# Kernel optimization log

Hardware: AMD Instinct MI355X
Metric: run time of the kernel (lower is better)

## Reference

```python
import jax, jax.numpy as jnp
import numpy as np

B, L, H, N, CH = 8, 2048, 512, 64, 1


def setup_inputs() -> dict:
    key = jax.random.key(0)
    ks = jax.random.split(key, 7)
    # S4D-Lin style init: w = -0.5 + i*pi*n, with slight noise on the real part
    w_re = -(0.5 + 0.1 * jax.random.uniform(ks[0], (H, N), dtype=jnp.float32))
    w_im = jnp.broadcast_to(jnp.pi * jnp.arange(N, dtype=jnp.float32), (H, N)).copy()
    C_re = jax.random.normal(ks[1], (CH, H, N), dtype=jnp.float32)
    C_im = jax.random.normal(ks[2], (CH, H, N), dtype=jnp.float32)
    D = jax.random.normal(ks[3], (CH, H), dtype=jnp.float32)
    # log-uniform dt in [1e-3, 1e-1]
    log_dt = jax.random.uniform(ks[4], (H,), dtype=jnp.float32,
                                minval=jnp.log(1e-3), maxval=jnp.log(1e-1))
    dt = jnp.exp(log_dt)
    u = jax.random.normal(ks[5], (B, L, H), dtype=jnp.float32)
    return {"u": u, "w_re": w_re, "w_im": w_im, "C_re": C_re,
            "C_im": C_im, "D": D, "dt": dt}


def reference(u, w_re, w_im, C_re, C_im, D, dt):
    # u: [B, L, H] -> [B, H, L]
    uT = jnp.swapaxes(u, -1, -2)
    l = uT.shape[-1]
    h = dt.shape[-1]
    w = (w_re + 1j * w_im).astype(jnp.complex64)          # [t, n]
    v = h // w.shape[0]
    w = jnp.tile(w, (v, 1))                                # [h, n]
    C = (C_re + 1j * C_im).astype(jnp.complex64)           # [c, h, n]
    # --- kernel generation ---
    dtA = w * dt[:, None]                                  # [h, n]
    K = jnp.arange(l) * dtA[..., None]                     # [h, n, l]
    Cs = C * ((jnp.exp(dtA) - 1.0) / w)                    # [c, h, n]
    k = 2.0 * jnp.einsum('chn,hnl->chl', Cs, jnp.exp(K)).real  # [c, h, l]
    # --- FFT convolution ---
    k_f = jnp.fft.rfft(k, n=2 * l - 1)                     # [c, h, l]
    u_f = jnp.fft.rfft(uT, n=2 * l - 1)                    # [B, h, l]
    y_f = jnp.einsum('...hl,chl->...chl', u_f, k_f)        # [B, c, h, l]
    y = jnp.fft.irfft(y_f, n=2 * l)[..., :l]               # [B, c, h, l]
    # skip connection
    y = y + jnp.einsum('...hl,ch->...chl', uT, D)
    # '... c h l -> ... l c h'
    return jnp.moveaxis(y, (-3, -2, -1), (-2, -1, -3))
```

## Files before the change

### kernel.cpp

```cpp
#include <hip/hip_runtime.h>
#include <hip/hip_bf16.h>
#include <math.h>


namespace {
constexpr int cB = 8;
constexpr int cL = 2048;
constexpr int cH = 512;
constexpr int cN = 64;
constexpr int M1 = 4095;
constexpr int M2 = 4096;
constexpr int BH = cB * cH;
constexpr int MA = BH + cH;

constexpr size_t S0   = 2 * ((size_t)cH * cN * 6);
constexpr size_t S_B1 = S0;
constexpr size_t S_A  = S_B1 + (size_t)4096 * 2048;
constexpr size_t S_T2 = S_A  + (size_t)MA * 2048;
constexpr size_t S_U  = S_T2 + (size_t)2048 * 4096;
}

typedef __attribute__((ext_vector_type(8))) short short8;
typedef __attribute__((ext_vector_type(4))) short sh4;
typedef __attribute__((ext_vector_type(4))) float f32x4;

static __device__ inline short f2bf(float x) {
    __hip_bfloat16 h = __float2bfloat16(x);
    return *reinterpret_cast<short*>(&h);
}
static __device__ inline float bf2f(short s) {
    return __uint_as_float(((unsigned int)(unsigned short)s) << 16);
}
static __device__ __forceinline__ void load_lds16(const short* g, short* l) {
    __builtin_amdgcn_global_load_lds(
        (const __attribute__((address_space(1))) void*)g,
        (__attribute__((address_space(3))) void*)l, 16, 0, 0);
}
#define WAIT_LGKM0() do { asm volatile("s_waitcnt lgkmcnt(0)" ::: "memory"); \
                          __builtin_amdgcn_sched_barrier(0); } while (0)
#define WAIT_VM(n)   do { asm volatile("s_waitcnt vmcnt(" #n ")" ::: "memory"); \
                          __builtin_amdgcn_sched_barrier(0); } while (0)
#define BAR() __builtin_amdgcn_s_barrier()

__global__ __launch_bounds__(256) void k_tabs(short* __restrict__ Wb)
{
    int tid = threadIdx.x;
    if (blockIdx.x < 2048) {
        int j  = blockIdx.x;
        int t0 = tid * 8;
        int p0 = (int)(((long)j * t0) % M1);
        float c, s, cs, ss;
        sincosf((6.283185307179586f / (float)M1) * (float)p0, &s, &c);
        sincosf((6.283185307179586f / (float)M1) * (float)j,  &ss, &cs);
        short8 vc, vs;
#pragma unroll
        for (int i = 0; i < 8; ++i) {
            vc[i] = f2bf(c); vs[i] = f2bf(s);
            float tr = c * cs - s * ss;
            s = c * ss + s * cs;
            c = tr;
        }
        *(short8*)&Wb[S_B1 + (size_t)(2 * j)     * 2048 + t0] = vc;
        *(short8*)&Wb[S_B1 + (size_t)(2 * j + 1) * 2048 + t0] = vs;
    } else {
        int t  = blockIdx.x - 2048;
        int j0 = tid * 8;
        int p0 = (t * j0) & (M2 - 1);
        float c, s, cs, ss;
        sincosf((6.283185307179586f / (float)M2) * (float)p0, &s, &c);
        sincosf((6.283185307179586f / (float)M2) * (float)t,  &ss, &cs);
        short8 vc, vs;
#pragma unroll
        for (int i = 0; i < 8; ++i) {
            vc[i] = f2bf(c); vs[i] = f2bf(s);
            float tr = c * cs - s * ss;
            s = c * ss + s * cs;
            c = tr;
        }
        *(short8*)&Wb[S_T2 + (size_t)t * 4096 + j0]        = vc;
        *(short8*)&Wb[S_T2 + (size_t)t * 4096 + 2048 + j0] = vs;
    }
}

__global__ __launch_bounds__(256) void k_trans(const float* __restrict__ u,
                                               short* __restrict__ Wb)
{
    __shared__ float tile[64][65];
    int t0 = blockIdx.x * 64;
    int h0 = blockIdx.y * 64;
    int b  = blockIdx.z;
    int cx = threadIdx.x & 63, r0 = threadIdx.x >> 6;
#pragma unroll
    for (int i = 0; i < 16; ++i) {
        int row = r0 + i * 4;
        tile[row][cx] = u[((size_t)b * cL + t0 + row) * cH + h0 + cx];
    }
    __syncthreads();
    short* A = Wb + S_A;
#pragma unroll
    for (int i = 0; i < 16; ++i) {
        int hrow = r0 + i * 4;
        A[(size_t)(b * cH + h0 + hrow) * 2048 + t0 + cx] = f2bf(tile[cx][hrow]);
    }
}

__global__ __launch_bounds__(256) void k_kgen(
    const float* __restrict__ w_re, const float* __restrict__ w_im,
    const float* __restrict__ C_re, const float* __restrict__ C_im,
    const float* __restrict__ dt, short* __restrict__ Wb)
{
    __shared__ float md[cN * 6];
    int h = blockIdx.x, tid = threadIdx.x;
    if (tid < cN) {
        int idx = h * cN + tid;
        double dtv = dt[h];
        double wr = w_re[idx], wi = w_im[idx];
        double ar = wr * dtv, ai = wi * dtv;
        double er = exp(ar);
        double zs, zc; sincos(ai, &zs, &zc);
        double zr = er * zc, zi = er * zs;
        double nr = zr - 1.0, ni = zi;
        double inv = 1.0 / (wr * wr + wi * wi);
        double gr = (nr * wr + ni * wi) * inv;
        double gi = (ni * wr - nr * wi) * inv;
        double cr = C_re[idx], ci = C_im[idx];
        md[tid*6+0] = (float)(cr * gr - ci * gi);
        md[tid*6+1] = (float)(cr * gi + ci * gr);
        md[tid*6+2] = (float)zr; md[tid*6+3] = (float)zi;
        md[tid*6+4] = (float)ar; md[tid*6+5] = (float)ai;
    }
    __syncthreads();
    int t0 = tid * 8;
    float acc[8] = {0.f, 0.f, 0.f, 0.f, 0.f, 0.f, 0.f, 0.f};
    for (int n = 0; n < cN; ++n) {
        float csr = md[n*6+0], csi = md[n*6+1];
        float zr  = md[n*6+2], zi  = md[n*6+3];
        float ar  = md[n*6+4], ai  = md[n*6+5];
        float mag = expf(ar * (float)t0);
        double ph = fmod((double)ai * (double)t0, 6.283185307179586);
        float s, c; sincosf((float)ph, &s, &c);
        float pr = mag * c, pi = mag * s;
#pragma unroll
        for (int i = 0; i < 8; ++i) {
            acc[i] += csr * pr - csi * pi;
            float tr = pr * zr - pi * zi;
            pi = pr * zi + pi * zr;
            pr = tr;
        }
    }
    short8 v;
#pragma unroll
    for (int i = 0; i < 8; ++i) v[i] = f2bf(2.f * acc[i]);
    *reinterpret_cast<short8*>(&Wb[S_A + (size_t)(BH + h) * 2048 + t0]) = v;
}

#define MFMA16(AR, BR, ACC) \
    _Pragma("unroll") for (int kk = 0; kk < 2; ++kk) \
    _Pragma("unroll") for (int ni = 0; ni < 2; ++ni) \
    _Pragma("unroll") for (int mi = 0; mi < 4; ++mi) \
        ACC[mi][ni] = __builtin_amdgcn_mfma_f32_16x16x32_bf16(AR[mi][kk], BR[ni][kk], ACC[mi][ni], 0, 0, 0);

__device__ __forceinline__ void gemm8p_core(
    const short* __restrict__ Ag, int lda,
    const short* __restrict__ Bg, int ldb,
    int m0, int n0, int nt, short* lds, f32x4 (&acc)[4][4][2])
{
    const int tid  = threadIdx.x;
    const int wave = tid >> 6, lane = tid & 63;
    const int wm = wave >> 2, wn = wave & 3;
    const int lm = lane & 15, lk = lane >> 4;
    const int srow8 = lane >> 3;
    const int scol  = (lane & 7) * 8;

    auto stage = [&](const short* G, int ldg, int row0, int half, int kt, int sb) {
        short* l0 = lds + sb + (size_t)((kt & 1) * 2 + half) * 8192;
#pragma unroll
        for (int q = 0; q < 2; ++q) {
            int chunk = wave * 2 + q;
            int r = chunk * 8 + srow8;
            int c = scol ^ ((r & 7) << 3);
            load_lds16(G + (size_t)(row0 + half * 128 + r) * ldg + kt * 64 + c,
                       l0 + chunk * 512);
        }
    };
    auto rdA = [&](int qa, int kt, int mi, int kk) -> short8 {
        int rl = wm * 64 + mi * 16 + lm;
        int c  = (kk * 32 + lk * 8) ^ ((rl & 7) << 3);
        return *(const short8*)(lds + (size_t)((kt & 1) * 2 + qa) * 8192 + rl * 64 + c);
    };
    auto rdB = [&](int qb, int kt, int ni, int kk) -> short8 {
        int rl = wn * 32 + ni * 16 + lm;
        int c  = (kk * 32 + lk * 8) ^ ((rl & 7) << 3);
        return *(const short8*)(lds + 32768 + (size_t)((kt & 1) * 2 + qb) * 8192 + rl * 64 + c);
    };

    stage(Ag, lda, m0, 0, 0, 0);
    stage(Bg, ldb, n0, 0, 0, 32768);
    stage(Bg, ldb, n0, 1, 0, 32768);
    stage(Ag, lda, m0, 1, 0, 0);
    stage(Ag, lda, m0, 0, 1, 0);
    stage(Bg, ldb, n0, 0, 1, 32768);
    stage(Bg, ldb, n0, 1, 1, 32768);
    stage(Ag, lda, m0, 1, 1, 0);
    WAIT_VM(12);
    BAR();

    short8 a0[4][2], a1[4][2], b0[2][2], b1[2][2];
    for (int t = 0; t < nt; ++t) {
        const bool st = (t + 2 < nt);
#pragma unroll
        for (int mi = 0; mi < 4; ++mi) { a0[mi][0] = rdA(0, t, mi, 0); a0[mi][1] = rdA(0, t, mi, 1); }
#pragma unroll
        for (int ni = 0; ni < 2; ++ni) { b0[ni][0] = rdB(0, t, ni, 0); b0[ni][1] = rdB(0, t, ni, 1); }
        BAR();
        WAIT_LGKM0();
        __builtin_amdgcn_s_setprio(1);
        MFMA16(a0, b0, acc[0]);
        __builtin_amdgcn_s_setprio(0);
        if (st) { WAIT_VM(10); } else { WAIT_VM(0); }
        BAR();
#pragma unroll
        for (int ni = 0; ni < 2; ++ni) { b1[ni][0] = rdB(1, t, ni, 0); b1[ni][1] = rdB(1, t, ni, 1); }
        if (st) { stage(Ag, lda, m0, 0, t + 2, 0); stage(Bg, ldb, n0, 0, t + 2, 32768); }
        BAR();
        WAIT_LGKM0();
        __builtin_amdgcn_s_setprio(1);
        MFMA16(a0, b1, acc[1]);
        __builtin_amdgcn_s_setprio(0);
        if (st) { WAIT_VM(12); } else { WAIT_VM(0); }
        BAR();
#pragma unroll
        for (int mi = 0; mi < 4; ++mi) { a1[mi][0] = rdA(1, t, mi, 0); a1[mi][1] = rdA(1, t, mi, 1); }
        if (st) stage(Bg, ldb, n0, 1, t + 2, 32768);
        BAR();
        WAIT_LGKM0();
        __builtin_amdgcn_s_setprio(1);
        MFMA16(a1, b1, acc[3]);
        __builtin_amdgcn_s_setprio(0);
        BAR();
        if (st) stage(Ag, lda, m0, 1, t + 2, 0);
        __builtin_amdgcn_s_setprio(1);
        MFMA16(a1, b0, acc[2]);
        __builtin_amdgcn_s_setprio(0);
        if (st) { WAIT_VM(12); } else { WAIT_VM(0); }
        BAR();
    }
}

__global__ __launch_bounds__(512, 2) void k_fwd8(short* __restrict__ Wb)
{
    __shared__ short lds_s[65536];
    int tile = (blockIdx.x & 7) * 32 + (blockIdx.x >> 3);
    const int m0 = (tile >> 4) * 256, n0 = (tile & 15) * 256;
    const int tid = threadIdx.x;
    const int wave = tid >> 6, lane = tid & 63;
    const int wm = wave >> 2, wn = wave & 3;
    const int lm = lane & 15, lk = lane >> 4;

    f32x4 acc[4][4][2] = {};
    gemm8p_core(Wb + S_A, 2048, Wb + S_B1, 2048, m0, n0, 32, lds_s, acc);

    short* Ys = Wb + S_U;
    const short* KF = Wb + S_U;
    short (*M)[136] = (short(*)[136])lds_s;
    for (int q = 0; q < 4; ++q) {
        __syncthreads();
#pragma unroll
        for (int mi = 0; mi < 4; ++mi)
#pragma unroll
        for (int ni = 0; ni < 2; ++ni)
#pragma unroll
        for (int r = 0; r < 4; ++r)
            M[wm * 64 + mi * 16 + lk * 4 + r][wn * 32 + ni * 16 + lm] =
                f2bf(acc[q][mi][ni][r]);
        __syncthreads();
        const int jwin = (n0 >> 1) + (q & 1) * 64;
#pragma unroll
        for (int pass = 0; pass < 4; ++pass) {
            int rl = pass * 32 + (tid >> 4);
            int p0 = (tid & 15) * 4;
            int rowg = m0 + (q >> 1) * 128 + rl;
            int h = rowg & (cH - 1);
            short8 kf8 = *(const short8*)&KF[(size_t)(4096 + h) * 4096 + 2 * (jwin + p0)];
            short8 m8  = *(const short8*)&M[rl][2 * p0];
            sh4 yr4, yi4;
#pragma unroll
            for (int i = 0; i < 4; ++i) {
                float C  = bf2f(m8[2*i]),  S  = bf2f(m8[2*i+1]);
                float Ck = bf2f(kf8[2*i]), Sk = bf2f(kf8[2*i+1]);
                int j = jwin + p0 + i;
                float sc = (j == 0 ? 1.0f : 2.0f) * (1.0f / (float)M2);
                yr4[i] = f2bf(sc * (Ck * C - Sk * S));
                yi4[i] = f2bf(sc * (Ck * S + Sk * C));
            }
            *(sh4*)&Ys[(size_t)rowg * 4096 + jwin + p0]        = yr4;
            *(sh4*)&Ys[(size_t)rowg * 4096 + 2048 + jwin + p0] = yi4;
        }
    }
}

__global__ __launch_bounds__(256, 2) void k_kfg(short* __restrict__ Wb)
{
    __shared__ __align__(16) short As[128][32];
    __shared__ __align__(16) short Bs[128][32];
    const short* A = Wb + S_A;
    const short* B = Wb + S_B1;
    short* U = Wb + S_U;
    const int tid = threadIdx.x;
    const int m0 = 4096 + blockIdx.y * 128, n0 = blockIdx.x * 128;
    const int wave = tid >> 6, lane = tid & 63;
    const int wr = wave >> 1, wc = wave & 1;
    const int lm = lane & 15, lk = lane >> 4;
    const int srow = lane >> 2, scol = (lane & 3) * 8;

    f32x4 acc[4][4] = {};
    for (int k0 = 0; k0 < 2048; k0 += 32) {
        __syncthreads();
        {
            int c0 = wave * 2;
            load_lds16(&A[(size_t)(m0 + c0*16      + srow)*2048 + k0 + scol], &As[c0*16][0]);
            load_lds16(&A[(size_t)(m0 + c0*16 + 16 + srow)*2048 + k0 + scol], &As[c0*16+16][0]);
            load_lds16(&B[(size_t)(n0 + c0*16      + srow)*2048 + k0 + scol], &Bs[c0*16][0]);
            load_lds16(&B[(size_t)(n0 + c0*16 + 16 + srow)*2048 + k0 + scol], &Bs[c0*16+16][0]);
        }
        __syncthreads();
        short8 a[4];
#pragma unroll
        for (int mi = 0; mi < 4; ++mi)
            a[mi] = *(const short8*)&As[wr*64 + mi*16 + lm][lk*8];
#pragma unroll
        for (int ni = 0; ni < 4; ++ni) {
            short8 b = *(const short8*)&Bs[wc*64 + ni*16 + lm][lk*8];
#pragma unroll
            for (int mi = 0; mi < 4; ++mi)
                acc[mi][ni] = __builtin_amdgcn_mfma_f32_16x16x32_bf16(a[mi], b, acc[mi][ni], 0, 0, 0);
        }
    }
#pragma unroll
    for (int mi = 0; mi < 4; ++mi)
#pragma unroll
    for (int ni = 0; ni < 4; ++ni)
#pragma unroll
    for (int r = 0; r < 4; ++r) {
        int row = m0 + wr*64 + mi*16 + lk*4 + r;
        int col = n0 + wc*64 + ni*16 + lm;
        U[(size_t)row * 4096 + col] = f2bf(acc[mi][ni][r]);
    }
}

__global__ __launch_bounds__(512, 1) void k_invB(const float* __restrict__ u,
                                                 const float* __restrict__ Dp,
                                                 short* __restrict__ Wb,
                                                 float* __restrict__ out)
{
    __shared__ short lds_s[57344];
    int tile = (blockIdx.x & 7) * 32 + (blockIdx.x >> 3);
    const int m0 = (tile >> 4) * 256;
    const int n0 = (tile & 15) * 128;
    const int tid = threadIdx.x;
    const int wave = tid >> 6, lane = tid & 63;
    const int wm = wave >> 2, wn = wave & 3;
    const int lm = lane & 15, lk = lane >> 4;
    const int srow8 = lane >> 3;
    const int scol  = (lane & 7) * 8;
    constexpr int nt = 64;
    short* lds = lds_s;
    const short* Ag = Wb + S_U;
    const short* Bg = Wb + S_T2;

    auto stageA = [&](int half, int kt) {
        short* l0 = lds + (size_t)((kt & 1) * 2 + half) * 8192;
#pragma unroll
        for (int q = 0; q < 2; ++q) {
            int chunk = wave * 2 + q;
            int r = chunk * 8 + srow8;
            int c = scol ^ ((r & 7) << 3);
            load_lds16(Ag + (size_t)(m0 + half * 128 + r) * 4096 + kt * 64 + c,
                       l0 + chunk * 512);
        }
    };
    auto stageB = [&](int kt, int slot) {
        short* l0 = lds + 32768 + (size_t)slot * 8192;
#pragma unroll
        for (int q = 0; q < 2; ++q) {
            int chunk = wave * 2 + q;
            int r = chunk * 8 + srow8;
            int c = scol ^ ((r & 7) << 3);
            load_lds16(Bg + (size_t)(n0 + r) * 4096 + kt * 64 + c,
                       l0 + chunk * 512);
        }
    };
    auto rdA = [&](int half, int kt, int mi, int kk) -> short8 {
        int rl = wm * 64 + mi * 16 + lm;
        int c  = (kk * 32 + lk * 8) ^ ((rl & 7) << 3);
        return *(const short8*)(lds + (size_t)((kt & 1) * 2 + half) * 8192 + rl * 64 + c);
    };
    auto rdB = [&](int slot, int ni, int kk) -> short8 {
        int rl = wn * 32 + ni * 16 + lm;
        int c  = (kk * 32 + lk * 8) ^ ((rl & 7) << 3);
        return *(const short8*)(lds + 32768 + (size_t)slot * 8192 + rl * 64 + c);
    };

    f32x4 acc[2][4][2] = {};

    stageA(0, 0);
    stageB(0, 0);
    stageA(1, 0);
    stageA(0, 1);
    stageB(1, 1);
    stageB(2, 2);
    WAIT_VM(6);
    BAR();

    short8 a[4][2], b[2][2];
    int bs = 0;
    for (int t = 0; t < nt; ++t) {
        const bool deep = (t + 3 < nt);
#pragma unroll
        for (int mi = 0; mi < 4; ++mi) { a[mi][0] = rdA(0, t, mi, 0); a[mi][1] = rdA(0, t, mi, 1); }
#pragma unroll
        for (int ni = 0; ni < 2; ++ni) { b[ni][0] = rdB(bs, ni, 0); b[ni][1] = rdB(bs, ni, 1); }
        if (t + 1 < nt) stageA(1, t + 1);
        BAR();
        WAIT_LGKM0();
        __builtin_amdgcn_s_setprio(1);
        MFMA16(a, b, acc[0]);
        __builtin_amdgcn_s_setprio(0);
        if (deep) { WAIT_VM(6); } else { WAIT_VM(0); }
        BAR();
#pragma unroll
        for (int mi = 0; mi < 4; ++mi) { a[mi][0] = rdA(1, t, mi, 0); a[mi][1] = rdA(1, t, mi, 1); }
        if (t + 2 < nt) stageA(0, t + 2);
        if (t + 3 < nt) stageB(t + 3, bs);
        BAR();
        WAIT_LGKM0();
        __builtin_amdgcn_s_setprio(1);
        MFMA16(a, b, acc[1]);
        __builtin_amdgcn_s_setprio(0);
        if (deep) { WAIT_VM(6); } else { WAIT_VM(0); }
        BAR();
        bs = (bs == 2) ? 0 : bs + 1;
    }

    const int b_  = m0 >> 9;
    const int h00 = m0 & 511;
    float (*T)[132] = (float(*)[132])lds_s;
#pragma unroll
    for (int q = 0; q < 2; ++q) {
        __syncthreads();
#pragma unroll
        for (int mi = 0; mi < 4; ++mi)
#pragma unroll
        for (int ni = 0; ni < 2; ++ni) {
            int tl = wn * 32 + ni * 16 + lm;
            int hl = wm * 64 + mi * 16 + lk * 4;
            *(float4*)&T[tl][hl] = *(float4*)&acc[q][mi][ni];
        }
        __syncthreads();
        int hg = h00 + q * 128 + (tid & 31) * 4;
        float4 dv = *(const float4*)&Dp[hg];
#pragma unroll
        for (int it = 0; it < 8; ++it) {
            int tl = (tid >> 5) + it * 16;
            int tg = n0 + tl;
            size_t gidx = ((size_t)b_ * cL + tg) * cH + hg;
            float4 uv = *(const float4*)&u[gidx];
            float4 yv = *(float4*)&T[tl][(tid & 31) * 4];
            yv.x += dv.x * uv.x;
            yv.y += dv.y * uv.y;
            yv.z += dv.z * uv.z;
            yv.w += dv.w * uv.w;
            *(float4*)&out[gidx] = yv;
        }
    }
}

extern "C" void kernel_launch(void* const* d_in, const int* in_sizes, int n_in,
                              void* d_out, int out_size, void* d_ws, size_t ws_size,
                              hipStream_t stream) {
    const float* u    = (const float*)d_in[0];
    const float* w_re = (const float*)d_in[1];
    const float* w_im = (const float*)d_in[2];
    const float* C_re = (const float*)d_in[3];
    const float* C_im = (const float*)d_in[4];
    const float* Dp   = (const float*)d_in[5];
    const float* dt   = (const float*)d_in[6];
    float* out = (float*)d_out;
    short* Wb  = (short*)d_ws;

    hipLaunchKernelGGL(k_tabs,  dim3(4096), dim3(256), 0, stream, Wb);
    hipLaunchKernelGGL(k_trans, dim3(cL / 64, cH / 64, cB), dim3(256), 0, stream, u, Wb);
    hipLaunchKernelGGL(k_kgen,  dim3(cH), dim3(256), 0, stream,
                       w_re, w_im, C_re, C_im, dt, Wb);
    hipLaunchKernelGGL(k_kfg,   dim3(32, 4), dim3(256), 0, stream, Wb);
    hipLaunchKernelGGL(k_fwd8,  dim3(256), dim3(512), 0, stream, Wb);
    hipLaunchKernelGGL(k_invB,  dim3(256), dim3(512), 0, stream, u, Dp, Wb, out);
}
```

Baseline: 232.1 us.

## Split inverse DFT into even/odd outputs using conjugate-symmetry folding

Adds a pass that folds each spectrum row into even/odd symmetric combinations (a+b, a-b) and rebuilds the inverse twiddle table as cos/sin halves per output parity. The inverse GEMM then uses K=2048 instead of 4096 for each parity, which halves its reduction length and total MACs. The cost is one extra kernel launch and an extra global round trip of the spectrum, and the extra bf16 rounding step may change accuracy slightly.

```diff
diff --git a/kernel.cpp b/kernel.cpp
--- a/kernel.cpp
+++ b/kernel.cpp
@@ -18,6 +18,7 @@
 constexpr size_t S_A  = S_B1 + (size_t)4096 * 2048;
 constexpr size_t S_T2 = S_A  + (size_t)MA * 2048;
 constexpr size_t S_U  = S_T2 + (size_t)2048 * 4096;
+constexpr size_t S_AP = S_B1;
 }
 
 typedef __attribute__((ext_vector_type(8))) short short8;
@@ -63,22 +64,37 @@
         *(short8*)&Wb[S_B1 + (size_t)(2 * j)     * 2048 + t0] = vc;
         *(short8*)&Wb[S_B1 + (size_t)(2 * j + 1) * 2048 + t0] = vs;
     } else {
-        int t  = blockIdx.x - 2048;
-        int j0 = tid * 8;
-        int p0 = (t * j0) & (M2 - 1);
-        float c, s, cs, ss;
-        sincosf((6.283185307179586f / (float)M2) * (float)p0, &s, &c);
-        sincosf((6.283185307179586f / (float)M2) * (float)t,  &ss, &cs);
-        short8 vc, vs;
-#pragma unroll
-        for (int i = 0; i < 8; ++i) {
-            vc[i] = f2bf(c); vs[i] = f2bf(s);
-            float tr = c * cs - s * ss;
-            s = c * ss + s * cs;
-            c = tr;
-        }
-        *(short8*)&Wb[S_T2 + (size_t)t * 4096 + j0]        = vc;
-        *(short8*)&Wb[S_T2 + (size_t)t * 4096 + 2048 + j0] = vs;
+        int r   = blockIdx.x - 2048;
+        int p   = r >> 10, tau = r & 1023;
+        int t   = 2 * tau + p;
+        int k0  = tid * 8;
+        float stepang = (6.283185307179586f / (float)M2) * (float)t;
+        float cs, ss; sincosf(stepang, &ss, &cs);
+        short8 v;
+        if (k0 < 1024) {
+            int ph = (k0 * t) & (M2 - 1);
+            float c, s; sincosf((6.283185307179586f / (float)M2) * (float)ph, &s, &c);
+#pragma unroll
+            for (int i = 0; i < 8; ++i) {
+                v[i] = f2bf(c);
+                float tr = c * cs - s * ss;
+                s = c * ss + s * cs;
+                c = tr;
+            }
+        } else {
+            int j0 = k0 - 1023;
+            int ph = (j0 * t) & (M2 - 1);
+            float c, s; sincosf((6.283185307179586f / (float)M2) * (float)ph, &s, &c);
+#pragma unroll
+            for (int i = 0; i < 8; ++i) {
+                int k = k0 + i;
+                v[i] = (k == 2047) ? f2bf((tau & 1) ? -1.f : 1.f) : f2bf(s);
+                float tr = c * cs - s * ss;
+                s = c * ss + s * cs;
+                c = tr;
+            }
+        }
+        *(short8*)&Wb[S_T2 + (size_t)r * 2048 + k0] = v;
     }
 }
 
@@ -348,6 +364,41 @@
     }
 }
 
+__global__ __launch_bounds__(256) void k_par(short* __restrict__ Wb)
+{
+    __shared__ short row[4096];
+    int bh = blockIdx.x, tid = threadIdx.x;
+    const short* Ysr = Wb + S_U + (size_t)bh * 4096;
+    *(short8*)&row[tid * 16]     = *(const short8*)&Ysr[tid * 16];
+    *(short8*)&row[tid * 16 + 8] = *(const short8*)&Ysr[tid * 16 + 8];
+    __syncthreads();
+    short* Ae = Wb + S_AP + (size_t)bh * 2048;
+    short* Ao = Wb + S_AP + (size_t)(4096 + bh) * 2048;
+    int k0 = tid * 8;
+    short8 ve, vo;
+#pragma unroll
+    for (int i = 0; i < 8; ++i) {
+        int k = k0 + i;
+        float e, o;
+        if (k == 0) {
+            e = o = bf2f(row[0]);
+        } else if (k < 1024) {
+            float a = bf2f(row[k]), b = bf2f(row[2048 - k]);
+            e = a + b; o = a - b;
+        } else if (k < 2047) {
+            int j = k - 1023;
+            float a = bf2f(row[2048 + j]), b = bf2f(row[4096 - j]);
+            e = a - b; o = a + b;
+        } else {
+            e = bf2f(row[1024]);
+            o = bf2f(row[2048 + 1024]);
+        }
+        ve[i] = f2bf(e); vo[i] = f2bf(o);
+    }
+    *(short8*)&Ae[k0] = ve;
+    *(short8*)&Ao[k0] = vo;
+}
+
 __global__ __launch_bounds__(512, 1) void k_invB(const float* __restrict__ u,
                                                  const float* __restrict__ Dp,
                                                  short* __restrict__ Wb,
@@ -355,18 +406,20 @@
 {
     __shared__ short lds_s[57344];
     int tile = (blockIdx.x & 7) * 32 + (blockIdx.x >> 3);
-    const int m0 = (tile >> 4) * 256;
-    const int n0 = (tile & 15) * 128;
+    const int m0   = (tile >> 4) * 256;
+    const int rest = tile & 15;
+    const int p    = rest >> 3;
+    const int n0   = (rest & 7) * 128;
     const int tid = threadIdx.x;
     const int wave = tid >> 6, lane = tid & 63;
     const int wm = wave >> 2, wn = wave & 3;
     const int lm = lane & 15, lk = lane >> 4;
     const int srow8 = lane >> 3;
     const int scol  = (lane & 7) * 8;
-    constexpr int nt = 64;
+    constexpr int nt = 32;
     short* lds = lds_s;
-    const short* Ag = Wb + S_U;
-    const short* Bg = Wb + S_T2;
+    const short* Ag = Wb + S_AP + (size_t)p * 4096 * 2048;
+    const short* Bg = Wb + S_T2 + (size_t)p * 1024 * 2048;
 
     auto stageA = [&](int half, int kt) {
         short* l0 = lds + (size_t)((kt & 1) * 2 + half) * 8192;
@@ -375,7 +428,7 @@
             int chunk = wave * 2 + q;
             int r = chunk * 8 + srow8;
             int c = scol ^ ((r & 7) << 3);
-            load_lds16(Ag + (size_t)(m0 + half * 128 + r) * 4096 + kt * 64 + c,
+            load_lds16(Ag + (size_t)(m0 + half * 128 + r) * 2048 + kt * 64 + c,
                        l0 + chunk * 512);
         }
     };
@@ -386,7 +439,7 @@
             int chunk = wave * 2 + q;
             int r = chunk * 8 + srow8;
             int c = scol ^ ((r & 7) << 3);
-            load_lds16(Bg + (size_t)(n0 + r) * 4096 + kt * 64 + c,
+            load_lds16(Bg + (size_t)(n0 + r) * 2048 + kt * 64 + c,
                        l0 + chunk * 512);
         }
     };
@@ -462,7 +515,7 @@
 #pragma unroll
         for (int it = 0; it < 8; ++it) {
             int tl = (tid >> 5) + it * 16;
-            int tg = n0 + tl;
+            int tg = 2 * (n0 + tl) + p;
             size_t gidx = ((size_t)b_ * cL + tg) * cH + hg;
             float4 uv = *(const float4*)&u[gidx];
             float4 yv = *(float4*)&T[tl][(tid & 31) * 4];
@@ -494,5 +547,6 @@
                        w_re, w_im, C_re, C_im, dt, Wb);
     hipLaunchKernelGGL(k_kfg,   dim3(32, 4), dim3(256), 0, stream, Wb);
     hipLaunchKernelGGL(k_fwd8,  dim3(256), dim3(512), 0, stream, Wb);
+    hipLaunchKernelGGL(k_par,   dim3(BH), dim3(256), 0, stream, Wb);
     hipLaunchKernelGGL(k_invB,  dim3(256), dim3(512), 0, stream, u, Dp, Wb, out);
 }
```

New measurement: 212.6 us. 1.09x faster.
